# Performance work log

Measured on AMD Instinct MI355X. Metric: run time of the kernel, lower is better.

The kernel has to match this reference:

```python
import jax, jax.numpy as jnp
import numpy as np

NUM_HEADS = 8
EMBED = 512
HEAD_DIM = EMBED // NUM_HEADS
B, S = 4, 2048


def setup_inputs() -> dict:
    key = jax.random.key(0)
    ks = jax.random.split(key, 8)
    sc = 0.02
    return {
        "values": jax.random.normal(ks[0], (B, S, EMBED), dtype=jnp.float32),
        "keys": jax.random.normal(ks[1], (B, S, EMBED), dtype=jnp.float32),
        "query": jax.random.normal(ks[2], (B, S, EMBED), dtype=jnp.float32),
        "Wv": jax.random.normal(ks[3], (HEAD_DIM, HEAD_DIM), dtype=jnp.float32) * sc,
        "Wk": jax.random.normal(ks[4], (HEAD_DIM, HEAD_DIM), dtype=jnp.float32) * sc,
        "Wq": jax.random.normal(ks[5], (HEAD_DIM, HEAD_DIM), dtype=jnp.float32) * sc,
        "Wo": jax.random.normal(ks[6], (EMBED, EMBED), dtype=jnp.float32) * sc,
        "bo": jnp.zeros((EMBED,), dtype=jnp.float32),
    }


def reference(values, keys, query, Wv, Wk, Wq, Wo, bo):
    b, s, _ = query.shape
    # split heads: [B, S, H, D]
    v = values.reshape(b, s, NUM_HEADS, HEAD_DIM)
    k = keys.reshape(b, s, NUM_HEADS, HEAD_DIM)
    q = query.reshape(b, s, NUM_HEADS, HEAD_DIM)
    # per-head linear (nn.Linear: x @ W.T), weights shared across heads
    v = jnp.einsum("bshd,ed->bshe", v, Wv)
    k = jnp.einsum("bshd,ed->bshe", k, Wk)
    q = jnp.einsum("bshd,ed->bshe", q, Wq)
    # energy: [B, H, Q, K]
    energy = jnp.einsum("bqhd,bkhd->bhqk", q, k)
    # NOTE: original scales by sqrt(embed_size), not sqrt(head_dim)
    attn = jax.nn.softmax(energy / jnp.sqrt(jnp.float32(EMBED)), axis=-1)
    out = jnp.einsum("bhqk,bkhd->bqhd", attn, v).reshape(b, s, EMBED)
    return out @ Wo.T + bo
```

## Files before the change

### kernel.cpp

```cpp
#include <hip/hip_runtime.h>

#define H 8
#define D 64
#define E 512
#define BATCH 4
#define SEQ 2048

typedef __bf16 bf16v8 __attribute__((ext_vector_type(8)));
typedef float f32v4 __attribute__((ext_vector_type(4)));
typedef unsigned int u32v4 __attribute__((ext_vector_type(4)));
typedef unsigned short u16v4 __attribute__((ext_vector_type(4)));

#define MFMA16(a,b,c) __builtin_amdgcn_mfma_f32_16x16x32_bf16(a,b,c,0,0,0)

#define AS1 __attribute__((address_space(1)))
#define AS3 __attribute__((address_space(3)))
#define GLDS16(g, l) __builtin_amdgcn_global_load_lds((const AS1 void*)(g), (AS3 void*)(l), 16, 0, 0)

static __device__ __forceinline__ unsigned short f2bf(float f) {
  unsigned u = __builtin_bit_cast(unsigned, f);
  u += 0x7fffu + ((u >> 16) & 1u);
  return (unsigned short)(u >> 16);
}

static __device__ __forceinline__ float exp2_hw(float x) {
#if __has_builtin(__builtin_amdgcn_exp2f)
  return __builtin_amdgcn_exp2f(x);
#else
  return exp2f(x);
#endif
}

static __device__ __forceinline__ bf16v8 lds16(const char* p) {
  return __builtin_bit_cast(bf16v8, *(const u32v4*)p);
}

static __device__ __forceinline__ unsigned cvtpk(float a, float b) {
  unsigned r;
  asm("v_cvt_pk_bf16_f32 %0, %1, %2" : "=v"(r) : "v"(a), "v"(b));
  return r;
}

__global__ void prep_all(const float* __restrict__ Wo, const float* __restrict__ Wv,
                         const float* __restrict__ Wq, const float* __restrict__ Wk,
                         const float* __restrict__ v, const float* __restrict__ keys,
                         unsigned short* __restrict__ Wo2, unsigned short* __restrict__ MT,
                         unsigned short* __restrict__ vT, unsigned short* __restrict__ kb) {
  __shared__ float tile[64][65];
  int bx = blockIdx.x;
  int t = threadIdx.x;
  if (bx < 1024) {
    int i = bx * 256 + t;
    int n = i >> 9, c = i & 511;
    int h = c >> 6, d = c & 63;
    float acc = 0.f;
    for (int e = 0; e < 64; ++e) acc += Wo[n*512 + h*64 + e] * Wv[e*64 + d];
    Wo2[n*512 + c] = f2bf(acc);
  } else if (bx < 1040) {
    int i = (bx - 1024) * 256 + t;
    int d2 = i >> 6, d1 = i & 63;
    float acc = 0.f;
    for (int e = 0; e < 64; ++e) acc += Wq[e*64 + d1] * Wk[e*64 + d2];
    MT[d2*64 + d1] = f2bf(acc * 0.04419417382415922f);
  } else {
    int flat = bx - 1040;
    int bh = flat >> 5, sc = flat & 31;
    int b = bh >> 3, h = bh & 7;
    {
      const float* kp = keys + (size_t)flat * 4096;
      unsigned short* ko = kb + (size_t)flat * 4096;
      #pragma unroll
      for (int i = 0; i < 4; ++i) {
        f32v4 x = *(const f32v4*)(kp + (i*256 + t)*4);
        u16v4 o = { f2bf(x[0]), f2bf(x[1]), f2bf(x[2]), f2bf(x[3]) };
        *(u16v4*)(ko + (i*256 + t)*4) = o;
      }
    }
    #pragma unroll
    for (int i = 0; i < 16; ++i) {
      int idx = i*256 + t; int si = idx >> 6, d = idx & 63;
      tile[si][d] = v[((size_t)(b*SEQ + sc*64 + si))*E + h*64 + d];
    }
    __syncthreads();
    #pragma unroll
    for (int i = 0; i < 16; ++i) {
      int idx = i*256 + t; int d = idx >> 6, si = idx & 63;
      vT[((size_t)(bh*64 + d))*SEQ + sc*64 + si] = f2bf(tile[si][d]);
    }
  }
}

__global__ __launch_bounds__(256, 2) void attn(const float* __restrict__ query,
                                               const unsigned short* __restrict__ MT,
                                               const unsigned short* __restrict__ kb,
                                               const unsigned short* __restrict__ vT,
                                               unsigned short* __restrict__ ao) {
  __shared__ __align__(16) char lds[40960];
  int bh = blockIdx.y, b = bh >> 3, h = bh & 7;
  int qt = blockIdx.x;
  int tid = threadIdx.x, w = tid >> 6, lane = tid & 63, hi = lane >> 4, lo = lane & 15;
  int b4 = hi & 1;

  const unsigned short* kbase = kb + (size_t)(b*SEQ)*E + h*64;
  const unsigned short* vbase = vT + (size_t)bh*64*SEQ;
  int srow = tid >> 3, scc = tid & 7;

  #pragma unroll
  for (int i = 0; i < 2; ++i) {
    int row = i*32 + srow;
    int sc = scc ^ (row & 7);
    GLDS16(kbase + (size_t)row*E + sc*8,   lds        + i*4096 + w*1024);
    GLDS16(vbase + (size_t)row*SEQ + sc*8, lds + 8192 + i*4096 + w*1024);
  }
  {
    char* xl = lds + 16384;
    char* ml = lds + 32768;
    #pragma unroll
    for (int i = 0; i < 8; ++i) {
      int c = i*256 + tid;
      int row = c >> 4, cc = c & 15;
      f32v4 xv = *(const f32v4*)(query + (size_t)(b*SEQ + qt*128 + row)*E + h*64 + cc*4);
      u16v4 o = { f2bf(xv[0]), f2bf(xv[1]), f2bf(xv[2]), f2bf(xv[3]) };
      int off = row*128 + ((((cc >> 1) ^ (row & 7))) << 4) + (cc & 1)*8;
      *(u16v4*)(xl + off) = o;
    }
    #pragma unroll
    for (int i = 0; i < 2; ++i) {
      int c = i*256 + tid; int row = c >> 3, cc = c & 7;
      *(u32v4*)(ml + row*128 + ((cc ^ (row & 7)) << 4)) = *(const u32v4*)(MT + row*64 + cc*8);
    }
  }
  __syncthreads();

  bf16v8 qa[2][2];
  {
    char* xl = lds + 16384;
    char* ml = lds + 32768;
    char* sq = lds + 16384 + w*4096;
    f32v4 qacc[2][4] = {};
    #pragma unroll
    for (int kk = 0; kk < 2; ++kk)
      #pragma unroll
      for (int mrep = 0; mrep < 2; ++mrep) {
        int arow = w*32 + mrep*16 + lo;
        bf16v8 af = lds16(xl + arow*128 + (((kk*4 + hi) ^ (arow & 7)) << 4));
        #pragma unroll
        for (int nt = 0; nt < 4; ++nt) {
          int brow = nt*16 + lo;
          bf16v8 bf_ = lds16(ml + brow*128 + (((kk*4 + hi) ^ (brow & 7)) << 4));
          qacc[mrep][nt] = MFMA16(af, bf_, qacc[mrep][nt]);
        }
      }
    #pragma unroll
    for (int mrep = 0; mrep < 2; ++mrep)
      #pragma unroll
      for (int nt = 0; nt < 4; ++nt)
        #pragma unroll
        for (int r = 0; r < 4; ++r) {
          int qrw = mrep*16 + 4*hi + r;
          *(unsigned short*)(sq + qrw*128 + ((nt*32 + lo*2) ^ ((qrw & 7) << 4))) =
              f2bf(qacc[mrep][nt][r]);
        }
    asm volatile("s_waitcnt lgkmcnt(0)" ::: "memory");
    __builtin_amdgcn_sched_barrier(0);
    #pragma unroll
    for (int mrep = 0; mrep < 2; ++mrep)
      #pragma unroll
      for (int kk = 0; kk < 2; ++kk) {
        int row = mrep*16 + lo;
        qa[mrep][kk] = lds16(sq + row*128 + (((kk*4 + hi) ^ (lo & 7)) << 4));
      }
  }
  __syncthreads();

  f32v4 oacc[2][4] = {};
  float lsum[2] = {0.f, 0.f};

  for (int kt = 0; kt < 32; ++kt) {
    const char* klc = lds + (kt & 1)*16384;
    const char* vlc = klc + 8192;
    if (kt < 31) {
      char* kln = lds + ((kt & 1) ^ 1)*16384;
      #pragma unroll
      for (int i = 0; i < 2; ++i) {
        int row = i*32 + srow;
        int sc = scc ^ (row & 7);
        GLDS16(kbase + (size_t)((kt+1)*64 + row)*E + sc*8, kln        + i*4096 + w*1024);
        GLDS16(vbase + (size_t)row*SEQ + (kt+1)*64 + sc*8, kln + 8192 + i*4096 + w*1024);
      }
    }
    f32v4 sacc[2][4] = {};
    __builtin_amdgcn_s_setprio(1);
    #pragma unroll
    for (int nt = 0; nt < 4; ++nt)
      #pragma unroll
      for (int kk = 0; kk < 2; ++kk) {
        int row = nt*16 + lo;
        bf16v8 kf = lds16(klc + row*128 + (((kk*4 + hi) ^ (row & 7)) << 4));
        sacc[0][nt] = MFMA16(kf, qa[0][kk], sacc[0][nt]);
        sacc[1][nt] = MFMA16(kf, qa[1][kk], sacc[1][nt]);
      }
    __builtin_amdgcn_s_setprio(0);
    unsigned wv[2][2][2][2];
    #pragma unroll
    for (int m = 0; m < 2; ++m)
      #pragma unroll
      for (int nt = 0; nt < 4; ++nt) {
        float p0 = exp2_hw(sacc[m][nt][0] * 1.4426950408889634f);
        float p1 = exp2_hw(sacc[m][nt][1] * 1.4426950408889634f);
        float p2 = exp2_hw(sacc[m][nt][2] * 1.4426950408889634f);
        float p3 = exp2_hw(sacc[m][nt][3] * 1.4426950408889634f);
        lsum[m] += (p0 + p1) + (p2 + p3);
        wv[m][nt >> 1][nt & 1][0] = cvtpk(p0, p1);
        wv[m][nt >> 1][nt & 1][1] = cvtpk(p2, p3);
      }
    #pragma unroll
    for (int m = 0; m < 2; ++m)
      #pragma unroll
      for (int nt1 = 0; nt1 < 2; ++nt1)
        #pragma unroll
        for (int s = 0; s < 2; ++s)
          asm("v_permlane32_swap_b32 %0, %1"
              : "+v"(wv[m][nt1][0][s]), "+v"(wv[m][nt1][1][s]));
    #pragma unroll
    for (int m = 0; m < 2; ++m)
      #pragma unroll
      for (int nt1 = 0; nt1 < 2; ++nt1)
        #pragma unroll
        for (int s = 0; s < 2; ++s) {
          int sent = b4 ? (int)wv[m][nt1][0][s] : (int)wv[m][nt1][1][s];
          unsigned recv = (unsigned)__shfl_xor(sent, 16);
          unsigned n0 = b4 ? recv : wv[m][nt1][0][s];
          unsigned n1 = b4 ? wv[m][nt1][1][s] : recv;
          wv[m][nt1][0][s] = n0;
          wv[m][nt1][1][s] = n1;
        }
    __builtin_amdgcn_s_setprio(1);
    #pragma unroll
    for (int ks = 0; ks < 2; ++ks) {
      u32v4 c0 = { wv[0][ks][0][0], wv[0][ks][0][1], wv[0][ks][1][0], wv[0][ks][1][1] };
      u32v4 c1 = { wv[1][ks][0][0], wv[1][ks][0][1], wv[1][ks][1][0], wv[1][ks][1][1] };
      bf16v8 pb0 = __builtin_bit_cast(bf16v8, c0);
      bf16v8 pb1 = __builtin_bit_cast(bf16v8, c1);
      #pragma unroll
      for (int dt = 0; dt < 4; ++dt) {
        int row = dt*16 + lo;
        bf16v8 vf = lds16(vlc + row*128 + (((ks*4 + hi) ^ (row & 7)) << 4));
        oacc[0][dt] = MFMA16(vf, pb0, oacc[0][dt]);
        oacc[1][dt] = MFMA16(vf, pb1, oacc[1][dt]);
      }
    }
    __builtin_amdgcn_s_setprio(0);
    __syncthreads();
  }
  #pragma unroll
  for (int m = 0; m < 2; ++m) {
    lsum[m] += __shfl_xor(lsum[m], 16);
    lsum[m] += __shfl_xor(lsum[m], 32);
    lsum[m] = __builtin_amdgcn_rcpf(lsum[m]);
  }
  #pragma unroll
  for (int m = 0; m < 2; ++m) {
    int tok = b*SEQ + qt*128 + w*32 + m*16 + lo;
    #pragma unroll
    for (int dt = 0; dt < 4; ++dt) {
      u16v4 o = { f2bf(oacc[m][dt][0] * lsum[m]), f2bf(oacc[m][dt][1] * lsum[m]),
                  f2bf(oacc[m][dt][2] * lsum[m]), f2bf(oacc[m][dt][3] * lsum[m]) };
      *(u16v4*)(ao + (size_t)tok*E + h*64 + dt*16 + 4*hi) = o;
    }
  }
}

__global__ __launch_bounds__(256, 2) void final_gemm(const unsigned short* __restrict__ ao,
                                                     const unsigned short* __restrict__ wo2,
                                                     const float* __restrict__ bo,
                                                     float* __restrict__ out) {
  __shared__ __align__(16) char lds[65536];
  int m0 = blockIdx.x * 128, n0 = blockIdx.y * 128;
  int tid = threadIdx.x, w = tid >> 6, lane = tid & 63, hi = lane >> 4, lo = lane & 15;
  int wm = (w >> 1) * 64, wn = (w & 1) * 64;
  int srow = tid >> 3, scc = tid & 7;
  f32v4 acc[4][4] = {};
  #pragma unroll
  for (int i = 0; i < 4; ++i) {
    int row = i*32 + srow;
    int sc = scc ^ (row & 7);
    GLDS16(ao  + (size_t)(m0 + row)*E + sc*8, lds         + i*4096 + w*1024);
    GLDS16(wo2 + (size_t)(n0 + row)*E + sc*8, lds + 16384 + i*4096 + w*1024);
  }
  __syncthreads();
  for (int kt = 0; kt < 8; ++kt) {
    const char* al = lds + (kt & 1)*32768;
    const char* bl = al + 16384;
    if (kt < 7) {
      char* an = lds + ((kt & 1) ^ 1)*32768;
      #pragma unroll
      for (int i = 0; i < 4; ++i) {
        int row = i*32 + srow;
        int sc = scc ^ (row & 7);
        GLDS16(ao  + (size_t)(m0 + row)*E + (kt+1)*64 + sc*8, an         + i*4096 + w*1024);
        GLDS16(wo2 + (size_t)(n0 + row)*E + (kt+1)*64 + sc*8, an + 16384 + i*4096 + w*1024);
      }
    }
    __builtin_amdgcn_s_setprio(1);
    #pragma unroll
    for (int kk = 0; kk < 2; ++kk) {
      bf16v8 af[4], bfv[4];
      #pragma unroll
      for (int mt = 0; mt < 4; ++mt) {
        int row = wm + mt*16 + lo;
        af[mt] = lds16(al + row*128 + (((kk*4 + hi) ^ (row & 7)) << 4));
      }
      #pragma unroll
      for (int nt = 0; nt < 4; ++nt) {
        int row = wn + nt*16 + lo;
        bfv[nt] = lds16(bl + row*128 + (((kk*4 + hi) ^ (row & 7)) << 4));
      }
      #pragma unroll
      for (int mt = 0; mt < 4; ++mt)
        #pragma unroll
        for (int nt = 0; nt < 4; ++nt)
          acc[mt][nt] = MFMA16(af[mt], bfv[nt], acc[mt][nt]);
    }
    __builtin_amdgcn_s_setprio(0);
    __syncthreads();
  }
  #pragma unroll
  for (int nt = 0; nt < 4; ++nt) {
    float bias = bo[n0 + wn + nt*16 + lo];
    #pragma unroll
    for (int mt = 0; mt < 4; ++mt)
      #pragma unroll
      for (int r = 0; r < 4; ++r)
        out[(size_t)(m0 + wm + mt*16 + 4*hi + r)*E + n0 + wn + nt*16 + lo] =
            acc[mt][nt][r] + bias;
  }
}

extern "C" void kernel_launch(void* const* d_in, const int* in_sizes, int n_in,
                              void* d_out, int out_size, void* d_ws, size_t ws_size,
                              hipStream_t stream) {
  const float* values = (const float*)d_in[0];
  const float* keys   = (const float*)d_in[1];
  const float* query  = (const float*)d_in[2];
  const float* Wv     = (const float*)d_in[3];
  const float* Wk     = (const float*)d_in[4];
  const float* Wq     = (const float*)d_in[5];
  const float* Wo     = (const float*)d_in[6];
  const float* bo     = (const float*)d_in[7];
  float* out = (float*)d_out;
  char* ws = (char*)d_ws;

  unsigned short* MT  = (unsigned short*)(ws);
  unsigned short* Wo2 = (unsigned short*)(ws + 8192);
  unsigned short* kb  = (unsigned short*)(ws + (1u  << 20));
  unsigned short* vT  = (unsigned short*)(ws + (9u  << 20));
  unsigned short* ao  = (unsigned short*)(ws + (17u << 20));

  prep_all  <<<2064, 256, 0, stream>>>(Wo, Wv, Wq, Wk, values, keys, Wo2, MT, vT, kb);
  attn      <<<dim3(16, 32), 256, 0, stream>>>(query, MT, kb, vT, ao);
  final_gemm<<<dim3(64, 4),  256, 0, stream>>>(ao, Wo2, bo, out);
}
```

Before: 163.9 us.

## Halve attention query tile, remap blocks, vectorize V transpose, shrink GEMM tiles

The attention kernel now handles 64 queries per block instead of 128, which doubles the grid to 1024 blocks. Launch bounds rise to 4 blocks per SM, and a block-index swizzle groups work items that share the same head. The Q projection now keeps results in registers, using permlane and shuffle exchanges instead of an LDS round-trip, and reads MT straight from global memory. The prep kernel's V transpose uses 16-byte vector loads and 8-byte stores, and the final GEMM uses 64x128 tiles so more blocks run at once. Together these aim to raise occupancy and parallelism, at the cost of reloading K/V tiles across twice as many attention blocks.

```diff
diff --git a/kernel.cpp b/kernel.cpp
--- a/kernel.cpp
+++ b/kernel.cpp
@@ -77,27 +77,32 @@
       }
     }
     #pragma unroll
-    for (int i = 0; i < 16; ++i) {
-      int idx = i*256 + t; int si = idx >> 6, d = idx & 63;
-      tile[si][d] = v[((size_t)(b*SEQ + sc*64 + si))*E + h*64 + d];
+    for (int i = 0; i < 4; ++i) {
+      int idx = i*256 + t; int si = idx >> 4, fc = (idx & 15)*4;
+      *(f32v4*)&tile[si][fc] =
+          *(const f32v4*)(v + (size_t)(b*SEQ + sc*64 + si)*E + h*64 + fc);
     }
     __syncthreads();
     #pragma unroll
-    for (int i = 0; i < 16; ++i) {
-      int idx = i*256 + t; int d = idx >> 6, si = idx & 63;
-      vT[((size_t)(bh*64 + d))*SEQ + sc*64 + si] = f2bf(tile[si][d]);
-    }
-  }
-}
-
-__global__ __launch_bounds__(256, 2) void attn(const float* __restrict__ query,
+    for (int i = 0; i < 4; ++i) {
+      int idx = i*256 + t; int d = idx >> 4, s4 = (idx & 15)*4;
+      u16v4 o = { f2bf(tile[s4+0][d]), f2bf(tile[s4+1][d]),
+                  f2bf(tile[s4+2][d]), f2bf(tile[s4+3][d]) };
+      *(u16v4*)(vT + (size_t)(bh*64 + d)*SEQ + sc*64 + s4) = o;
+    }
+  }
+}
+
+__global__ __launch_bounds__(256, 4) void attn(const float* __restrict__ query,
                                                const unsigned short* __restrict__ MT,
                                                const unsigned short* __restrict__ kb,
                                                const unsigned short* __restrict__ vT,
                                                unsigned short* __restrict__ ao) {
   __shared__ __align__(16) char lds[40960];
-  int bh = blockIdx.y, b = bh >> 3, h = bh & 7;
-  int qt = blockIdx.x;
+  int orig = blockIdx.x;
+  int workid = (orig & 7) * 128 + (orig >> 3);
+  int bh = workid >> 5, qt = workid & 31;
+  int b = bh >> 3, h = bh & 7;
   int tid = threadIdx.x, w = tid >> 6, lane = tid & 63, hi = lane >> 4, lo = lane & 15;
   int b4 = hi & 1;
 
@@ -113,68 +118,68 @@
     GLDS16(vbase + (size_t)row*SEQ + sc*8, lds + 8192 + i*4096 + w*1024);
   }
   {
-    char* xl = lds + 16384;
-    char* ml = lds + 32768;
-    #pragma unroll
-    for (int i = 0; i < 8; ++i) {
+    char* xl = lds + 32768;
+    #pragma unroll
+    for (int i = 0; i < 4; ++i) {
       int c = i*256 + tid;
       int row = c >> 4, cc = c & 15;
-      f32v4 xv = *(const f32v4*)(query + (size_t)(b*SEQ + qt*128 + row)*E + h*64 + cc*4);
+      f32v4 xv = *(const f32v4*)(query + (size_t)(b*SEQ + qt*64 + row)*E + h*64 + cc*4);
       u16v4 o = { f2bf(xv[0]), f2bf(xv[1]), f2bf(xv[2]), f2bf(xv[3]) };
       int off = row*128 + ((((cc >> 1) ^ (row & 7))) << 4) + (cc & 1)*8;
       *(u16v4*)(xl + off) = o;
     }
-    #pragma unroll
-    for (int i = 0; i < 2; ++i) {
-      int c = i*256 + tid; int row = c >> 3, cc = c & 7;
-      *(u32v4*)(ml + row*128 + ((cc ^ (row & 7)) << 4)) = *(const u32v4*)(MT + row*64 + cc*8);
-    }
   }
   __syncthreads();
 
-  bf16v8 qa[2][2];
+  bf16v8 qa[2];
   {
-    char* xl = lds + 16384;
-    char* ml = lds + 32768;
-    char* sq = lds + 16384 + w*4096;
-    f32v4 qacc[2][4] = {};
+    const char* xl = lds + 32768;
+    bf16v8 qrf[2];
+    #pragma unroll
+    for (int kk = 0; kk < 2; ++kk) {
+      int row = w*16 + lo;
+      qrf[kk] = lds16(xl + row*128 + (((kk*4 + hi) ^ (row & 7)) << 4));
+    }
+    f32v4 qacc[4] = {};
     #pragma unroll
     for (int kk = 0; kk < 2; ++kk)
       #pragma unroll
-      for (int mrep = 0; mrep < 2; ++mrep) {
-        int arow = w*32 + mrep*16 + lo;
-        bf16v8 af = lds16(xl + arow*128 + (((kk*4 + hi) ^ (arow & 7)) << 4));
-        #pragma unroll
-        for (int nt = 0; nt < 4; ++nt) {
-          int brow = nt*16 + lo;
-          bf16v8 bf_ = lds16(ml + brow*128 + (((kk*4 + hi) ^ (brow & 7)) << 4));
-          qacc[mrep][nt] = MFMA16(af, bf_, qacc[mrep][nt]);
-        }
-      }
-    #pragma unroll
-    for (int mrep = 0; mrep < 2; ++mrep)
-      #pragma unroll
-      for (int nt = 0; nt < 4; ++nt)
-        #pragma unroll
-        for (int r = 0; r < 4; ++r) {
-          int qrw = mrep*16 + 4*hi + r;
-          *(unsigned short*)(sq + qrw*128 + ((nt*32 + lo*2) ^ ((qrw & 7) << 4))) =
-              f2bf(qacc[mrep][nt][r]);
-        }
-    asm volatile("s_waitcnt lgkmcnt(0)" ::: "memory");
-    __builtin_amdgcn_sched_barrier(0);
-    #pragma unroll
-    for (int mrep = 0; mrep < 2; ++mrep)
-      #pragma unroll
-      for (int kk = 0; kk < 2; ++kk) {
-        int row = mrep*16 + lo;
-        qa[mrep][kk] = lds16(sq + row*128 + (((kk*4 + hi) ^ (lo & 7)) << 4));
-      }
-  }
-  __syncthreads();
-
-  f32v4 oacc[2][4] = {};
-  float lsum[2] = {0.f, 0.f};
+      for (int nt = 0; nt < 4; ++nt) {
+        bf16v8 mtf = *(const bf16v8*)(MT + (nt*16 + lo)*64 + kk*32 + hi*8);
+        qacc[nt] = MFMA16(mtf, qrf[kk], qacc[nt]);
+      }
+    unsigned qv[2][2][2];
+    #pragma unroll
+    for (int nt = 0; nt < 4; ++nt) {
+      qv[nt >> 1][nt & 1][0] = cvtpk(qacc[nt][0], qacc[nt][1]);
+      qv[nt >> 1][nt & 1][1] = cvtpk(qacc[nt][2], qacc[nt][3]);
+    }
+    #pragma unroll
+    for (int nt1 = 0; nt1 < 2; ++nt1)
+      #pragma unroll
+      for (int s = 0; s < 2; ++s)
+        asm("v_permlane32_swap_b32 %0, %1"
+            : "+v"(qv[nt1][0][s]), "+v"(qv[nt1][1][s]));
+    #pragma unroll
+    for (int nt1 = 0; nt1 < 2; ++nt1)
+      #pragma unroll
+      for (int s = 0; s < 2; ++s) {
+        int sent = b4 ? (int)qv[nt1][0][s] : (int)qv[nt1][1][s];
+        unsigned recv = (unsigned)__shfl_xor(sent, 16);
+        unsigned n0 = b4 ? recv : qv[nt1][0][s];
+        unsigned n1 = b4 ? qv[nt1][1][s] : recv;
+        qv[nt1][0][s] = n0;
+        qv[nt1][1][s] = n1;
+      }
+    #pragma unroll
+    for (int kk = 0; kk < 2; ++kk) {
+      u32v4 c0 = { qv[kk][0][0], qv[kk][0][1], qv[kk][1][0], qv[kk][1][1] };
+      qa[kk] = __builtin_bit_cast(bf16v8, c0);
+    }
+  }
+
+  f32v4 oacc[4] = {};
+  float lsum = 0.f;
 
   for (int kt = 0; kt < 32; ++kt) {
     const char* klc = lds + (kt & 1)*16384;
@@ -189,7 +194,7 @@
         GLDS16(vbase + (size_t)row*SEQ + (kt+1)*64 + sc*8, kln + 8192 + i*4096 + w*1024);
       }
     }
-    f32v4 sacc[2][4] = {};
+    f32v4 sacc[4] = {};
     __builtin_amdgcn_s_setprio(1);
     #pragma unroll
     for (int nt = 0; nt < 4; ++nt)
@@ -197,75 +202,61 @@
       for (int kk = 0; kk < 2; ++kk) {
         int row = nt*16 + lo;
         bf16v8 kf = lds16(klc + row*128 + (((kk*4 + hi) ^ (row & 7)) << 4));
-        sacc[0][nt] = MFMA16(kf, qa[0][kk], sacc[0][nt]);
-        sacc[1][nt] = MFMA16(kf, qa[1][kk], sacc[1][nt]);
+        sacc[nt] = MFMA16(kf, qa[kk], sacc[nt]);
       }
     __builtin_amdgcn_s_setprio(0);
-    unsigned wv[2][2][2][2];
-    #pragma unroll
-    for (int m = 0; m < 2; ++m)
-      #pragma unroll
-      for (int nt = 0; nt < 4; ++nt) {
-        float p0 = exp2_hw(sacc[m][nt][0] * 1.4426950408889634f);
-        float p1 = exp2_hw(sacc[m][nt][1] * 1.4426950408889634f);
-        float p2 = exp2_hw(sacc[m][nt][2] * 1.4426950408889634f);
-        float p3 = exp2_hw(sacc[m][nt][3] * 1.4426950408889634f);
-        lsum[m] += (p0 + p1) + (p2 + p3);
-        wv[m][nt >> 1][nt & 1][0] = cvtpk(p0, p1);
-        wv[m][nt >> 1][nt & 1][1] = cvtpk(p2, p3);
-      }
-    #pragma unroll
-    for (int m = 0; m < 2; ++m)
-      #pragma unroll
-      for (int nt1 = 0; nt1 < 2; ++nt1)
-        #pragma unroll
-        for (int s = 0; s < 2; ++s)
-          asm("v_permlane32_swap_b32 %0, %1"
-              : "+v"(wv[m][nt1][0][s]), "+v"(wv[m][nt1][1][s]));
-    #pragma unroll
-    for (int m = 0; m < 2; ++m)
-      #pragma unroll
-      for (int nt1 = 0; nt1 < 2; ++nt1)
-        #pragma unroll
-        for (int s = 0; s < 2; ++s) {
-          int sent = b4 ? (int)wv[m][nt1][0][s] : (int)wv[m][nt1][1][s];
-          unsigned recv = (unsigned)__shfl_xor(sent, 16);
-          unsigned n0 = b4 ? recv : wv[m][nt1][0][s];
-          unsigned n1 = b4 ? wv[m][nt1][1][s] : recv;
-          wv[m][nt1][0][s] = n0;
-          wv[m][nt1][1][s] = n1;
-        }
+    unsigned wv[2][2][2];
+    #pragma unroll
+    for (int nt = 0; nt < 4; ++nt) {
+      float p0 = exp2_hw(sacc[nt][0] * 1.4426950408889634f);
+      float p1 = exp2_hw(sacc[nt][1] * 1.4426950408889634f);
+      float p2 = exp2_hw(sacc[nt][2] * 1.4426950408889634f);
+      float p3 = exp2_hw(sacc[nt][3] * 1.4426950408889634f);
+      lsum += (p0 + p1) + (p2 + p3);
+      wv[nt >> 1][nt & 1][0] = cvtpk(p0, p1);
+      wv[nt >> 1][nt & 1][1] = cvtpk(p2, p3);
+    }
+    #pragma unroll
+    for (int nt1 = 0; nt1 < 2; ++nt1)
+      #pragma unroll
+      for (int s = 0; s < 2; ++s)
+        asm("v_permlane32_swap_b32 %0, %1"
+            : "+v"(wv[nt1][0][s]), "+v"(wv[nt1][1][s]));
+    #pragma unroll
+    for (int nt1 = 0; nt1 < 2; ++nt1)
+      #pragma unroll
+      for (int s = 0; s < 2; ++s) {
+        int sent = b4 ? (int)wv[nt1][0][s] : (int)wv[nt1][1][s];
+        unsigned recv = (unsigned)__shfl_xor(sent, 16);
+        unsigned n0 = b4 ? recv : wv[nt1][0][s];
+        unsigned n1 = b4 ? wv[nt1][1][s] : recv;
+        wv[nt1][0][s] = n0;
+        wv[nt1][1][s] = n1;
+      }
     __builtin_amdgcn_s_setprio(1);
     #pragma unroll
     for (int ks = 0; ks < 2; ++ks) {
-      u32v4 c0 = { wv[0][ks][0][0], wv[0][ks][0][1], wv[0][ks][1][0], wv[0][ks][1][1] };
-      u32v4 c1 = { wv[1][ks][0][0], wv[1][ks][0][1], wv[1][ks][1][0], wv[1][ks][1][1] };
-      bf16v8 pb0 = __builtin_bit_cast(bf16v8, c0);
-      bf16v8 pb1 = __builtin_bit_cast(bf16v8, c1);
+      u32v4 c0 = { wv[ks][0][0], wv[ks][0][1], wv[ks][1][0], wv[ks][1][1] };
+      bf16v8 pb = __builtin_bit_cast(bf16v8, c0);
       #pragma unroll
       for (int dt = 0; dt < 4; ++dt) {
         int row = dt*16 + lo;
         bf16v8 vf = lds16(vlc + row*128 + (((ks*4 + hi) ^ (row & 7)) << 4));
-        oacc[0][dt] = MFMA16(vf, pb0, oacc[0][dt]);
-        oacc[1][dt] = MFMA16(vf, pb1, oacc[1][dt]);
+        oacc[dt] = MFMA16(vf, pb, oacc[dt]);
       }
     }
     __builtin_amdgcn_s_setprio(0);
     __syncthreads();
   }
-  #pragma unroll
-  for (int m = 0; m < 2; ++m) {
-    lsum[m] += __shfl_xor(lsum[m], 16);
-    lsum[m] += __shfl_xor(lsum[m], 32);
-    lsum[m] = __builtin_amdgcn_rcpf(lsum[m]);
-  }
-  #pragma unroll
-  for (int m = 0; m < 2; ++m) {
-    int tok = b*SEQ + qt*128 + w*32 + m*16 + lo;
+  lsum += __shfl_xor(lsum, 16);
+  lsum += __shfl_xor(lsum, 32);
+  lsum = __builtin_amdgcn_rcpf(lsum);
+  {
+    int tok = b*SEQ + qt*64 + w*16 + lo;
     #pragma unroll
     for (int dt = 0; dt < 4; ++dt) {
-      u16v4 o = { f2bf(oacc[m][dt][0] * lsum[m]), f2bf(oacc[m][dt][1] * lsum[m]),
-                  f2bf(oacc[m][dt][2] * lsum[m]), f2bf(oacc[m][dt][3] * lsum[m]) };
+      u16v4 o = { f2bf(oacc[dt][0] * lsum), f2bf(oacc[dt][1] * lsum),
+                  f2bf(oacc[dt][2] * lsum), f2bf(oacc[dt][3] * lsum) };
       *(u16v4*)(ao + (size_t)tok*E + h*64 + dt*16 + 4*hi) = o;
     }
   }
@@ -275,39 +266,49 @@
                                                      const unsigned short* __restrict__ wo2,
                                                      const float* __restrict__ bo,
                                                      float* __restrict__ out) {
-  __shared__ __align__(16) char lds[65536];
-  int m0 = blockIdx.x * 128, n0 = blockIdx.y * 128;
+  __shared__ __align__(16) char lds[49152];
+  int m0 = blockIdx.x * 64, n0 = blockIdx.y * 128;
   int tid = threadIdx.x, w = tid >> 6, lane = tid & 63, hi = lane >> 4, lo = lane & 15;
-  int wm = (w >> 1) * 64, wn = (w & 1) * 64;
+  int wm = (w >> 1) * 32, wn = (w & 1) * 64;
   int srow = tid >> 3, scc = tid & 7;
-  f32v4 acc[4][4] = {};
+  f32v4 acc[2][4] = {};
+  #pragma unroll
+  for (int i = 0; i < 2; ++i) {
+    int row = i*32 + srow;
+    int sc = scc ^ (row & 7);
+    GLDS16(ao + (size_t)(m0 + row)*E + sc*8, lds + i*4096 + w*1024);
+  }
   #pragma unroll
   for (int i = 0; i < 4; ++i) {
     int row = i*32 + srow;
     int sc = scc ^ (row & 7);
-    GLDS16(ao  + (size_t)(m0 + row)*E + sc*8, lds         + i*4096 + w*1024);
-    GLDS16(wo2 + (size_t)(n0 + row)*E + sc*8, lds + 16384 + i*4096 + w*1024);
+    GLDS16(wo2 + (size_t)(n0 + row)*E + sc*8, lds + 8192 + i*4096 + w*1024);
   }
   __syncthreads();
   for (int kt = 0; kt < 8; ++kt) {
-    const char* al = lds + (kt & 1)*32768;
-    const char* bl = al + 16384;
+    const char* al = lds + (kt & 1)*24576;
+    const char* bl = al + 8192;
     if (kt < 7) {
-      char* an = lds + ((kt & 1) ^ 1)*32768;
+      char* an = lds + ((kt & 1) ^ 1)*24576;
+      #pragma unroll
+      for (int i = 0; i < 2; ++i) {
+        int row = i*32 + srow;
+        int sc = scc ^ (row & 7);
+        GLDS16(ao + (size_t)(m0 + row)*E + (kt+1)*64 + sc*8, an + i*4096 + w*1024);
+      }
       #pragma unroll
       for (int i = 0; i < 4; ++i) {
         int row = i*32 + srow;
         int sc = scc ^ (row & 7);
-        GLDS16(ao  + (size_t)(m0 + row)*E + (kt+1)*64 + sc*8, an         + i*4096 + w*1024);
-        GLDS16(wo2 + (size_t)(n0 + row)*E + (kt+1)*64 + sc*8, an + 16384 + i*4096 + w*1024);
+        GLDS16(wo2 + (size_t)(n0 + row)*E + (kt+1)*64 + sc*8, an + 8192 + i*4096 + w*1024);
       }
     }
     __builtin_amdgcn_s_setprio(1);
     #pragma unroll
     for (int kk = 0; kk < 2; ++kk) {
-      bf16v8 af[4], bfv[4];
-      #pragma unroll
-      for (int mt = 0; mt < 4; ++mt) {
+      bf16v8 af[2], bfv[4];
+      #pragma unroll
+      for (int mt = 0; mt < 2; ++mt) {
         int row = wm + mt*16 + lo;
         af[mt] = lds16(al + row*128 + (((kk*4 + hi) ^ (row & 7)) << 4));
       }
@@ -317,7 +318,7 @@
         bfv[nt] = lds16(bl + row*128 + (((kk*4 + hi) ^ (row & 7)) << 4));
       }
       #pragma unroll
-      for (int mt = 0; mt < 4; ++mt)
+      for (int mt = 0; mt < 2; ++mt)
         #pragma unroll
         for (int nt = 0; nt < 4; ++nt)
           acc[mt][nt] = MFMA16(af[mt], bfv[nt], acc[mt][nt]);
@@ -329,7 +330,7 @@
   for (int nt = 0; nt < 4; ++nt) {
     float bias = bo[n0 + wn + nt*16 + lo];
     #pragma unroll
-    for (int mt = 0; mt < 4; ++mt)
+    for (int mt = 0; mt < 2; ++mt)
       #pragma unroll
       for (int r = 0; r < 4; ++r)
         out[(size_t)(m0 + wm + mt*16 + 4*hi + r)*E + n0 + wn + nt*16 + lo] =
@@ -358,6 +359,6 @@
   unsigned short* ao  = (unsigned short*)(ws + (17u << 20));
 
   prep_all  <<<2064, 256, 0, stream>>>(Wo, Wv, Wq, Wk, values, keys, Wo2, MT, vT, kb);
-  attn      <<<dim3(16, 32), 256, 0, stream>>>(query, MT, kb, vT, ao);
-  final_gemm<<<dim3(64, 4),  256, 0, stream>>>(ao, Wo2, bo, out);
-}
+  attn      <<<1024, 256, 0, stream>>>(query, MT, kb, vT, ao);
+  final_gemm<<<dim3(128, 4), 256, 0, stream>>>(ao, Wo2, bo, out);
+}
```

Result: no change. 166.9 us (+1.9%).
